# Optimization experiments

Hardware: AMD Instinct MI355X
Metric: run time of the kernel (lower is better)

## Reference

```python
import jax, jax.numpy as jnp
from jax import lax
import numpy as np

WIDTH = 3.0        # tool half-width (voxels)
SIGMA = 1.0        # soft mask edge (voxels)
BLUR_SIGMA = 1.5   # post-deposit isotropic blur sigma (voxels)
EPS = 1e-8


def _gauss_blur(x, sigma):
    """Separable Gaussian blur over the last two axes of x: [B, X, Y]."""
    radius = int(3 * sigma)
    t = jnp.arange(-radius, radius + 1, dtype=x.dtype)
    k = jnp.exp(-0.5 * (t / sigma) ** 2)
    k = k / k.sum()
    x4 = x[:, None]                      # [B,1,X,Y] NCHW
    kh = k.reshape(1, 1, -1, 1)
    x4 = lax.conv_general_dilated(x4, kh, (1, 1), 'SAME')
    kw = k.reshape(1, 1, 1, -1)
    x4 = lax.conv_general_dilated(x4, kw, (1, 1), 'SAME')
    return x4[:, 0]


def setup_inputs() -> dict:
    key = jax.random.key(0)
    k1, k2, k3 = jax.random.split(key, 3)
    B, H, W = 16, 1024, 1024
    occ = jax.random.uniform(k1, (B, H, W), dtype=jnp.float32)
    # push start/end points well inside the grid (voxel coordinates)
    action_start = jax.random.uniform(k2, (B, 3), minval=200.0, maxval=800.0, dtype=jnp.float32)
    action_end = action_start + jax.random.uniform(k3, (B, 3), minval=-150.0, maxval=150.0, dtype=jnp.float32)
    return {"occ": occ, "action_start": action_start, "action_end": action_end}


def reference(occ, action_start, action_end):
    # coordinate-convention transpose (see SplatPushModel docs)
    rho = jnp.swapaxes(occ, 1, 2)            # [B, X, Y]
    B, X, Y = rho.shape
    p0 = action_start[:, :2]                 # [B,2]
    p1 = action_end[:, :2]                   # [B,2]

    d = p1 - p0
    L = jnp.sqrt(jnp.sum(d * d, axis=-1) + EPS)      # [B] segment length
    u = d / L[:, None]                               # unit push direction
    n = jnp.stack([-u[:, 1], u[:, 0]], axis=-1)      # unit normal

    gx = jnp.arange(X, dtype=rho.dtype)[None, :, None]   # [1,X,1]
    gy = jnp.arange(Y, dtype=rho.dtype)[None, None, :]   # [1,1,Y]
    bc = lambda v: v[:, None, None]                      # [B] -> [B,1,1]

    # --- swept band: soft distance-to-segment mask ---
    rx = gx - bc(p0[:, 0])
    ry = gy - bc(p0[:, 1])
    t = jnp.clip(rx * bc(u[:, 0]) + ry * bc(u[:, 1]), 0.0, L[:, None, None])
    dx = rx - t * bc(u[:, 0])
    dy = ry - t * bc(u[:, 1])
    dist = jnp.sqrt(dx * dx + dy * dy + EPS)
    swept = jax.nn.sigmoid((WIDTH - dist) / SIGMA)       # [B,X,Y]

    m_swept = jnp.sum(rho * swept, axis=(1, 2))          # [B] mass to move
    pile_depth = m_swept / (2.0 * WIDTH)                 # [B]

    # --- landing zone probe (rectangle past p1) ---
    qx = gx - bc(p1[:, 0])
    qy = gy - bc(p1[:, 1])
    s = qx * bc(u[:, 0]) + qy * bc(u[:, 1])              # along-direction coord
    r = qx * bc(n[:, 0]) + qy * bc(n[:, 1])              # perpendicular coord
    lat = jax.nn.sigmoid((WIDTH - jnp.abs(r)) / SIGMA)
    probe = jax.nn.sigmoid(s / SIGMA) * jax.nn.sigmoid((bc(pile_depth) - s) / SIGMA) * lat
    existing = jnp.sum(rho * probe, axis=(1, 2))         # [B]
    extra = existing / (2.0 * WIDTH)                     # [B] forward extension

    # --- deposit band, shifted forward by extra_depth ---
    dep_mask = (jax.nn.sigmoid((s - bc(extra)) / SIGMA)
                * jax.nn.sigmoid((bc(extra) + bc(pile_depth) - s) / SIGMA)
                * lat)
    dep_norm = m_swept / (jnp.sum(dep_mask, axis=(1, 2)) + EPS)
    dep = dep_mask * dep_norm[:, None, None]             # mass-conserving deposit

    if BLUR_SIGMA > 0:
        dep = _gauss_blur(dep, BLUR_SIGMA)

    rho_new = rho * (1.0 - swept) + dep
    return jnp.swapaxes(rho_new, 1, 2)
```

## Files before the change

kernel.cpp:

```cpp
#include <hip/hip_runtime.h>
#include <math.h>

#define BB    16
#define HH    1024
#define WW    1024
#define EPSF  1e-8f
#define RAD   4
#define MARG  24.f
#define WMAX  128
#define FW    (WMAX + 16)
#define UNR   4

struct BlurK { float k[9]; };

__device__ __forceinline__ float sigf(float z) {
    z = fmaxf(fminf(z, 40.f), -40.f);
    return 1.f / (1.f + __expf(-z));
}

struct Geom { float p0x, p0y, p1x, p1y, L, ux, uy; };

__device__ __forceinline__ Geom load_geom(const float* as, const float* ae, int b) {
    Geom g;
    g.p0x = as[3 * b];  g.p0y = as[3 * b + 1];
    g.p1x = ae[3 * b];  g.p1y = ae[3 * b + 1];
    float dx = g.p1x - g.p0x, dy = g.p1y - g.p0y;
    g.L  = sqrtf(dx * dx + dy * dy + EPSF);
    g.ux = dx / g.L;  g.uy = dy / g.L;
    return g;
}

__device__ __forceinline__ float sweptf(const Geom& g, float x, float y) {
    float rx = x - g.p0x, ry = y - g.p0y;
    float t  = fminf(fmaxf(rx * g.ux + ry * g.uy, 0.f), g.L);
    float dx = rx - t * g.ux, dy = ry - t * g.uy;
    float dist = sqrtf(dx * dx + dy * dy + EPSF);
    return sigf(3.f - dist);
}

__device__ __forceinline__ void slat(const Geom& g, float x, float y, float& s, float& lat) {
    float qx = x - g.p1x, qy = y - g.p1y;
    s = qx * g.ux + qy * g.uy;
    float r = qx * (-g.uy) + qy * g.ux;
    lat = sigf(3.f - fabsf(r));
}

__device__ __forceinline__ void capsule_bbox(const Geom& g, float m,
                                             int& x0, int& x1, int& y0, int& y1) {
    x0 = max(0, (int)floorf(fminf(g.p0x, g.p1x) - m));
    x1 = min(WW - 1, (int)ceilf(fmaxf(g.p0x, g.p1x) + m));
    y0 = max(0, (int)floorf(fminf(g.p0y, g.p1y) - m));
    y1 = min(HH - 1, (int)ceilf(fmaxf(g.p0y, g.p1y) + m));
}

__device__ __forceinline__ void strip_bbox(const Geom& g, float s0, float s1, float m,
                                           int& x0, int& x1, int& y0, int& y1) {
    float xmin = 1e9f, xmax = -1e9f, ymin = 1e9f, ymax = -1e9f;
    #pragma unroll
    for (int i = 0; i < 4; i++) {
        float s = (i & 1) ? s1 : s0;
        float r = (i & 2) ? m : -m;
        float x = g.p1x + s * g.ux - r * g.uy;
        float y = g.p1y + s * g.uy + r * g.ux;
        xmin = fminf(xmin, x); xmax = fmaxf(xmax, x);
        ymin = fminf(ymin, y); ymax = fmaxf(ymax, y);
    }
    x0 = max(0, (int)floorf(xmin)); x1 = min(WW - 1, (int)ceilf(xmax));
    y0 = max(0, (int)floorf(ymin)); y1 = min(HH - 1, (int)ceilf(ymax));
}

__device__ __forceinline__ bool ivx(float a, float A, float B, float& lo, float& hi) {
    if (fabsf(a) < 1e-5f) return !(A > 0.f || B < 0.f);
    float l = A / a, h = B / a;
    if (a < 0.f) { float t = l; l = h; h = t; }
    lo = fmaxf(lo, l); hi = fminf(hi, h);
    return true;
}

__device__ __forceinline__ float brb1024(float v, float* sm) {
    #pragma unroll
    for (int off = 32; off > 0; off >>= 1) v += __shfl_down(v, off);
    const int lane = threadIdx.x & 63, wid = threadIdx.x >> 6;
    if (lane == 0) sm[wid] = v;
    __syncthreads();
    float r = 0.f;
    #pragma unroll
    for (int i = 0; i < 16; i++) r += sm[i];
    __syncthreads();
    return r;
}

__global__ __launch_bounds__(1024)
void k_scalars(const float* __restrict__ occ, const float* __restrict__ as,
               const float* __restrict__ ae, float* __restrict__ sc) {
    const int b = blockIdx.x, tid = threadIdx.x;
    const int tx4 = tid & 63;
    const int ty  = tid >> 6;
    __shared__ float sm[16];
    Geom g = load_geom(as, ae, b);
    const float4* src4 = (const float4*)(occ + ((size_t)b << 20));

    int x0, x1, y0, y1;

    capsule_bbox(g, MARG, x0, x1, y0, y1);
    int c0 = x0 >> 2, c1 = x1 >> 2;
    float sum = 0.f;
    for (int cc = c0; cc <= c1; cc += 64) {
        const int c = cc + tx4;
        const bool cok = (c <= c1);
        const float fx = (float)(c << 2);
        for (int y = y0 + ty; y <= y1; y += 16 * UNR) {
            float4 vv[UNR];
            #pragma unroll
            for (int j = 0; j < UNR; j++) {
                const int yy = y + 16 * j;
                vv[j] = (cok && yy <= y1) ? src4[yy * 256 + c]
                                          : make_float4(0.f, 0.f, 0.f, 0.f);
            }
            #pragma unroll
            for (int j = 0; j < UNR; j++) {
                const int yy = y + 16 * j;
                if (cok && yy <= y1) {
                    const float fy = (float)yy;
                    sum += vv[j].x * sweptf(g, fx + 0.f, fy);
                    sum += vv[j].y * sweptf(g, fx + 1.f, fy);
                    sum += vv[j].z * sweptf(g, fx + 2.f, fy);
                    sum += vv[j].w * sweptf(g, fx + 3.f, fy);
                }
            }
        }
    }
    const float m_swept = brb1024(sum, sm);
    const float pile = m_swept * (1.f / 6.f);

    strip_bbox(g, -MARG, pile + MARG, MARG, x0, x1, y0, y1);
    c0 = x0 >> 2; c1 = x1 >> 2;
    sum = 0.f;
    for (int cc = c0; cc <= c1; cc += 64) {
        const int c = cc + tx4;
        const bool cok = (c <= c1);
        const float fx = (float)(c << 2);
        for (int y = y0 + ty; y <= y1; y += 16 * UNR) {
            float4 vv[UNR];
            #pragma unroll
            for (int j = 0; j < UNR; j++) {
                const int yy = y + 16 * j;
                vv[j] = (cok && yy <= y1) ? src4[yy * 256 + c]
                                          : make_float4(0.f, 0.f, 0.f, 0.f);
            }
            #pragma unroll
            for (int j = 0; j < UNR; j++) {
                const int yy = y + 16 * j;
                if (cok && yy <= y1) {
                    const float fy = (float)yy;
                    #pragma unroll
                    for (int e = 0; e < 4; e++) {
                        float s, lat; slat(g, fx + (float)e, fy, s, lat);
                        sum += (&vv[j].x)[e] * sigf(s) * sigf(pile - s) * lat;
                    }
                }
            }
        }
    }
    const float existing = brb1024(sum, sm);
    const float extra = existing * (1.f / 6.f);

    strip_bbox(g, extra - MARG, extra + pile + MARG, MARG, x0, x1, y0, y1);
    sum = 0.f;
    {
        const int tx = tid & 127, ty8 = tid >> 7;
        for (int y = y0 + ty8; y <= y1; y += 8) {
            const float fy = (float)y;
            for (int x = x0 + tx; x <= x1; x += 128) {
                float s, lat; slat(g, (float)x, fy, s, lat);
                sum += sigf(s - extra) * sigf(extra + pile - s) * lat;
            }
        }
    }
    const float summask = brb1024(sum, sm);

    if (tid == 0) {
        sc[b * 4 + 0] = pile;
        sc[b * 4 + 1] = extra;
        sc[b * 4 + 2] = m_swept / (summask + EPSF);
    }
}

__global__ __launch_bounds__(256)
void k_fused(const float* __restrict__ occ, const float* __restrict__ as,
             const float* __restrict__ ae, const float* __restrict__ sc,
             float* __restrict__ out, BlurK wk) {
    const int b = blockIdx.y, bx = blockIdx.x, tid = threadIdx.x;
    const float pile     = sc[b * 4 + 0];
    const float extra    = sc[b * 4 + 1];
    const float dep_norm = sc[b * 4 + 2];
    Geom g = load_geom(as, ae, b);

    const size_t ibase = (size_t)b << 20;
    const float4* src = (const float4*)(occ + ibase);
    float4*       dst = (float4*)(out + ibase);
    const int yb = bx * 8;
    const int base4 = bx * 2048 + tid;

    float4 v[8];
    #pragma unroll
    for (int k = 0; k < 8; k++) v[k] = src[base4 + k * 256];

    int cx0, cx1, cy0, cy1; capsule_bbox(g, MARG, cx0, cx1, cy0, cy1);
    const int x = tid << 2;
    if (x + 3 >= cx0 && x <= cx1) {
        #pragma unroll
        for (int k = 0; k < 8; k++) {
            const int y = yb + k;
            if (y >= cy0 && y <= cy1) {
                const float fy = (float)y, fx = (float)x;
                v[k].x *= 1.f - sweptf(g, fx + 0.f, fy);
                v[k].y *= 1.f - sweptf(g, fx + 1.f, fy);
                v[k].z *= 1.f - sweptf(g, fx + 2.f, fy);
                v[k].w *= 1.f - sweptf(g, fx + 3.f, fy);
            }
        }
    }

    int sx0, sx1, sy0, sy1;
    strip_bbox(g, extra - MARG, extra + pile + MARG, MARG, sx0, sx1, sy0, sy1);

    __shared__ float draw[16][FW];
    __shared__ float hb[16][WMAX];

    if (yb + 7 >= sy0 && yb <= sy1) {
        const float sA = extra - MARG, sB = extra + pile + MARG;
        float xlo = 1e9f, xhi = -1e9f;
        #pragma unroll
        for (int r = 0; r < 16; r++) {
            const float dy = (float)(yb - RAD + r) - g.p1y;
            float lo = -1e9f, hi = 1e9f;
            bool ok = ivx(g.ux, sA - dy * g.uy, sB - dy * g.uy, lo, hi);
            ok = ok && ivx(-g.uy, -MARG - dy * g.ux, MARG - dy * g.ux, lo, hi);
            if (ok && lo <= hi) { xlo = fminf(xlo, lo); xhi = fmaxf(xhi, hi); }
        }
        const int csx0 = max(sx0, (int)floorf(xlo + g.p1x));
        const int csx1 = min(sx1, (int)ceilf(xhi + g.p1x));

        if (csx0 <= csx1) {
            const int cxa = csx0 & ~3;
            for (int cx = cxa; cx <= csx1; cx += WMAX) {
                const int w = min(WMAX, csx1 - cx + 1);

                for (int i = tid; i < 16 * FW; i += 256) {
                    const int ly = i / FW, lx = i - ly * FW;
                    if (lx < w + 8) {
                        const int gy = yb - RAD + ly, gx = cx - RAD + lx;
                        float val = 0.f;
                        if ((unsigned)gx < WW && (unsigned)gy < HH) {
                            float s, lat; slat(g, (float)gx, (float)gy, s, lat);
                            val = sigf(s - extra) * sigf(extra + pile - s) * lat * dep_norm;
                        }
                        draw[ly][lx] = val;
                    }
                }
                __syncthreads();

                for (int i = tid; i < 16 * WMAX; i += 256) {
                    const int ly = i >> 7, lx = i & 127;
                    if (lx < w) {
                        float acc = 0.f;
                        #pragma unroll
                        for (int j = 0; j < 9; j++) acc += wk.k[j] * draw[ly][lx + j];
                        hb[ly][lx] = acc;
                    }
                }
                __syncthreads();

                for (int i = tid; i < 8 * WMAX; i += 256) {
                    const int k = i >> 7, lx = i & 127;
                    if (lx < w) {
                        float acc = 0.f;
                        #pragma unroll
                        for (int j = 0; j < 9; j++) acc += wk.k[j] * hb[k + j][lx];
                        draw[k][lx] = acc;
                    }
                }
                __syncthreads();

                const int lx0 = (tid << 2) - cx;
                if (lx0 >= 0 && lx0 < w) {
                    if (lx0 + 3 < w) {
                        #pragma unroll
                        for (int k = 0; k < 8; k++) {
                            const float4 vb = *(const float4*)&draw[k][lx0];
                            v[k].x += vb.x; v[k].y += vb.y; v[k].z += vb.z; v[k].w += vb.w;
                        }
                    } else {
                        #pragma unroll
                        for (int k = 0; k < 8; k++)
                            for (int e = 0; e < 4; e++)
                                if (lx0 + e < w) (&v[k].x)[e] += draw[k][lx0 + e];
                    }
                }
                __syncthreads();
            }
        }
    }

    #pragma unroll
    for (int k = 0; k < 8; k++) dst[base4 + k * 256] = v[k];
}

extern "C" void kernel_launch(void* const* d_in, const int* in_sizes, int n_in,
                              void* d_out, int out_size, void* d_ws, size_t ws_size,
                              hipStream_t stream) {
    const float* occ = (const float*)d_in[0];
    const float* as  = (const float*)d_in[1];
    const float* ae  = (const float*)d_in[2];
    float* out = (float*)d_out;
    float* sc  = (float*)d_ws;

    BlurK wk;
    {
        float s = 0.f;
        for (int i = 0; i < 9; i++) {
            float t = (float)(i - RAD) / 1.5f;
            wk.k[i] = expf(-0.5f * t * t);
            s += wk.k[i];
        }
        for (int i = 0; i < 9; i++) wk.k[i] /= s;
    }

    k_scalars<<<dim3(BB), 1024, 0, stream>>>(occ, as, ae, sc);
    k_fused  <<<dim3(HH / 8, BB), 256, 0, stream>>>(occ, as, ae, sc, out, wk);
}
```

Measured before the change: 163.3 us.

## Fuse swept-mass reduction into streaming pass and split deposit into sparse kernel

The main streaming kernel now copies occ to out, applies the swept mask, and produces per-block partial sums of swept mass in the same pass. This removes the serial swept-mass reduction from the 16-block scalar kernel, which now only runs the probe and mask-sum phases. The blur and deposit move to a separate small kernel that adds into out only over the strip bbox tiles. The cost is an extra launch and a read-modify-write of the deposit region in global memory.

```diff
diff --git a/kernel.cpp b/kernel.cpp
--- a/kernel.cpp
+++ b/kernel.cpp
@@ -7,6 +7,8 @@
 #define EPSF  1e-8f
 #define RAD   4
 #define MARG  24.f
+#define NB1   128
+#define NB3   32
 #define WMAX  128
 #define FW    (WMAX + 16)
 #define UNR   4
@@ -77,6 +79,17 @@
     return true;
 }
 
+__device__ __forceinline__ float brb256(float v, float* sm) {
+    #pragma unroll
+    for (int off = 32; off > 0; off >>= 1) v += __shfl_down(v, off);
+    const int lane = threadIdx.x & 63, wid = threadIdx.x >> 6;
+    if (lane == 0) sm[wid] = v;
+    __syncthreads();
+    float r = sm[0] + sm[1] + sm[2] + sm[3];
+    __syncthreads();
+    return r;
+}
+
 __device__ __forceinline__ float brb1024(float v, float* sm) {
     #pragma unroll
     for (int off = 32; off > 0; off >>= 1) v += __shfl_down(v, off);
@@ -90,9 +103,53 @@
     return r;
 }
 
+__global__ __launch_bounds__(256)
+void k_main(const float* __restrict__ occ, const float* __restrict__ as,
+            const float* __restrict__ ae, float* __restrict__ out,
+            float* __restrict__ part1) {
+    const int b = blockIdx.y, bx = blockIdx.x, tid = threadIdx.x;
+    Geom g = load_geom(as, ae, b);
+    const size_t ibase = (size_t)b << 20;
+    const float4* src = (const float4*)(occ + ibase);
+    float4*       dst = (float4*)(out + ibase);
+    const int yb = bx * 8;
+    const int base4 = bx * 2048 + tid;
+
+    float4 v[8];
+    #pragma unroll
+    for (int k = 0; k < 8; k++) v[k] = src[base4 + k * 256];
+
+    int cx0, cx1, cy0, cy1; capsule_bbox(g, MARG, cx0, cx1, cy0, cy1);
+    const int x = tid << 2;
+    float msum = 0.f;
+    if (x + 3 >= cx0 && x <= cx1) {
+        #pragma unroll
+        for (int k = 0; k < 8; k++) {
+            const int y = yb + k;
+            if (y >= cy0 && y <= cy1) {
+                const float fy = (float)y, fx = (float)x;
+                const float s0 = sweptf(g, fx + 0.f, fy);
+                const float s1 = sweptf(g, fx + 1.f, fy);
+                const float s2 = sweptf(g, fx + 2.f, fy);
+                const float s3 = sweptf(g, fx + 3.f, fy);
+                msum += v[k].x * s0 + v[k].y * s1 + v[k].z * s2 + v[k].w * s3;
+                v[k].x *= 1.f - s0; v[k].y *= 1.f - s1;
+                v[k].z *= 1.f - s2; v[k].w *= 1.f - s3;
+            }
+        }
+    }
+    #pragma unroll
+    for (int k = 0; k < 8; k++) dst[base4 + k * 256] = v[k];
+
+    __shared__ float sm[4];
+    const float bs = brb256(msum, sm);
+    if (tid == 0) part1[b * NB1 + bx] = bs;
+}
+
 __global__ __launch_bounds__(1024)
-void k_scalars(const float* __restrict__ occ, const float* __restrict__ as,
-               const float* __restrict__ ae, float* __restrict__ sc) {
+void k_probe(const float* __restrict__ occ, const float* __restrict__ as,
+             const float* __restrict__ ae, const float* __restrict__ part1,
+             float* __restrict__ sc) {
     const int b = blockIdx.x, tid = threadIdx.x;
     const int tx4 = tid & 63;
     const int ty  = tid >> 6;
@@ -100,9 +157,11 @@
     Geom g = load_geom(as, ae, b);
     const float4* src4 = (const float4*)(occ + ((size_t)b << 20));
 
+    const float m_swept = brb1024((tid < NB1) ? part1[b * NB1 + tid] : 0.f, sm);
+    const float pile = m_swept * (1.f / 6.f);
+
     int x0, x1, y0, y1;
-
-    capsule_bbox(g, MARG, x0, x1, y0, y1);
+    strip_bbox(g, -MARG, pile + MARG, MARG, x0, x1, y0, y1);
     int c0 = x0 >> 2, c1 = x1 >> 2;
     float sum = 0.f;
     for (int cc = c0; cc <= c1; cc += 64) {
@@ -122,37 +181,6 @@
                 const int yy = y + 16 * j;
                 if (cok && yy <= y1) {
                     const float fy = (float)yy;
-                    sum += vv[j].x * sweptf(g, fx + 0.f, fy);
-                    sum += vv[j].y * sweptf(g, fx + 1.f, fy);
-                    sum += vv[j].z * sweptf(g, fx + 2.f, fy);
-                    sum += vv[j].w * sweptf(g, fx + 3.f, fy);
-                }
-            }
-        }
-    }
-    const float m_swept = brb1024(sum, sm);
-    const float pile = m_swept * (1.f / 6.f);
-
-    strip_bbox(g, -MARG, pile + MARG, MARG, x0, x1, y0, y1);
-    c0 = x0 >> 2; c1 = x1 >> 2;
-    sum = 0.f;
-    for (int cc = c0; cc <= c1; cc += 64) {
-        const int c = cc + tx4;
-        const bool cok = (c <= c1);
-        const float fx = (float)(c << 2);
-        for (int y = y0 + ty; y <= y1; y += 16 * UNR) {
-            float4 vv[UNR];
-            #pragma unroll
-            for (int j = 0; j < UNR; j++) {
-                const int yy = y + 16 * j;
-                vv[j] = (cok && yy <= y1) ? src4[yy * 256 + c]
-                                          : make_float4(0.f, 0.f, 0.f, 0.f);
-            }
-            #pragma unroll
-            for (int j = 0; j < UNR; j++) {
-                const int yy = y + 16 * j;
-                if (cok && yy <= y1) {
-                    const float fy = (float)yy;
                     #pragma unroll
                     for (int e = 0; e < 4; e++) {
                         float s, lat; slat(g, fx + (float)e, fy, s, lat);
@@ -187,53 +215,32 @@
 }
 
 __global__ __launch_bounds__(256)
-void k_fused(const float* __restrict__ occ, const float* __restrict__ as,
-             const float* __restrict__ ae, const float* __restrict__ sc,
-             float* __restrict__ out, BlurK wk) {
+void k_dep(const float* __restrict__ as, const float* __restrict__ ae,
+           const float* __restrict__ sc, float* __restrict__ out, BlurK wk) {
     const int b = blockIdx.y, bx = blockIdx.x, tid = threadIdx.x;
     const float pile     = sc[b * 4 + 0];
     const float extra    = sc[b * 4 + 1];
     const float dep_norm = sc[b * 4 + 2];
     Geom g = load_geom(as, ae, b);
 
-    const size_t ibase = (size_t)b << 20;
-    const float4* src = (const float4*)(occ + ibase);
-    float4*       dst = (float4*)(out + ibase);
-    const int yb = bx * 8;
-    const int base4 = bx * 2048 + tid;
-
-    float4 v[8];
-    #pragma unroll
-    for (int k = 0; k < 8; k++) v[k] = src[base4 + k * 256];
-
-    int cx0, cx1, cy0, cy1; capsule_bbox(g, MARG, cx0, cx1, cy0, cy1);
-    const int x = tid << 2;
-    if (x + 3 >= cx0 && x <= cx1) {
-        #pragma unroll
-        for (int k = 0; k < 8; k++) {
-            const int y = yb + k;
-            if (y >= cy0 && y <= cy1) {
-                const float fy = (float)y, fx = (float)x;
-                v[k].x *= 1.f - sweptf(g, fx + 0.f, fy);
-                v[k].y *= 1.f - sweptf(g, fx + 1.f, fy);
-                v[k].z *= 1.f - sweptf(g, fx + 2.f, fy);
-                v[k].w *= 1.f - sweptf(g, fx + 3.f, fy);
-            }
-        }
-    }
-
     int sx0, sx1, sy0, sy1;
     strip_bbox(g, extra - MARG, extra + pile + MARG, MARG, sx0, sx1, sy0, sy1);
+    if (sx0 > sx1 || sy0 > sy1) return;
+    float* outb = out + ((size_t)b << 20);
 
     __shared__ float draw[16][FW];
     __shared__ float hb[16][WMAX];
 
-    if (yb + 7 >= sy0 && yb <= sy1) {
-        const float sA = extra - MARG, sB = extra + pile + MARG;
+    const int nty = (sy1 - sy0) / 8 + 1;
+    const float sA = extra - MARG, sB = extra + pile + MARG;
+
+    for (int ty = bx; ty < nty; ty += NB3) {
+        const int yt = sy0 + ty * 8;
+
         float xlo = 1e9f, xhi = -1e9f;
         #pragma unroll
         for (int r = 0; r < 16; r++) {
-            const float dy = (float)(yb - RAD + r) - g.p1y;
+            const float dy = (float)(yt - RAD + r) - g.p1y;
             float lo = -1e9f, hi = 1e9f;
             bool ok = ivx(g.ux, sA - dy * g.uy, sB - dy * g.uy, lo, hi);
             ok = ok && ivx(-g.uy, -MARG - dy * g.ux, MARG - dy * g.ux, lo, hi);
@@ -241,70 +248,56 @@
         }
         const int csx0 = max(sx0, (int)floorf(xlo + g.p1x));
         const int csx1 = min(sx1, (int)ceilf(xhi + g.p1x));
-
-        if (csx0 <= csx1) {
-            const int cxa = csx0 & ~3;
-            for (int cx = cxa; cx <= csx1; cx += WMAX) {
-                const int w = min(WMAX, csx1 - cx + 1);
-
-                for (int i = tid; i < 16 * FW; i += 256) {
-                    const int ly = i / FW, lx = i - ly * FW;
-                    if (lx < w + 8) {
-                        const int gy = yb - RAD + ly, gx = cx - RAD + lx;
-                        float val = 0.f;
-                        if ((unsigned)gx < WW && (unsigned)gy < HH) {
-                            float s, lat; slat(g, (float)gx, (float)gy, s, lat);
-                            val = sigf(s - extra) * sigf(extra + pile - s) * lat * dep_norm;
-                        }
-                        draw[ly][lx] = val;
+        if (csx0 > csx1) continue;
+
+        for (int cx = csx0 & ~3; cx <= csx1; cx += WMAX) {
+            const int w = min(WMAX, csx1 - cx + 1);
+
+            for (int i = tid; i < 16 * FW; i += 256) {
+                const int ly = i / FW, lx = i - ly * FW;
+                if (lx < w + 8) {
+                    const int gy = yt - RAD + ly, gx = cx - RAD + lx;
+                    float val = 0.f;
+                    if ((unsigned)gx < WW && (unsigned)gy < HH) {
+                        float s, lat; slat(g, (float)gx, (float)gy, s, lat);
+                        val = sigf(s - extra) * sigf(extra + pile - s) * lat * dep_norm;
                     }
+                    draw[ly][lx] = val;
                 }
-                __syncthreads();
-
-                for (int i = tid; i < 16 * WMAX; i += 256) {
-                    const int ly = i >> 7, lx = i & 127;
-                    if (lx < w) {
-                        float acc = 0.f;
-                        #pragma unroll
-                        for (int j = 0; j < 9; j++) acc += wk.k[j] * draw[ly][lx + j];
-                        hb[ly][lx] = acc;
-                    }
+            }
+            __syncthreads();
+
+            for (int i = tid; i < 16 * WMAX; i += 256) {
+                const int ly = i >> 7, lx = i & 127;
+                if (lx < w) {
+                    float acc = 0.f;
+                    #pragma unroll
+                    for (int j = 0; j < 9; j++) acc += wk.k[j] * draw[ly][lx + j];
+                    hb[ly][lx] = acc;
                 }
-                __syncthreads();
-
-                for (int i = tid; i < 8 * WMAX; i += 256) {
-                    const int k = i >> 7, lx = i & 127;
-                    if (lx < w) {
-                        float acc = 0.f;
-                        #pragma unroll
-                        for (int j = 0; j < 9; j++) acc += wk.k[j] * hb[k + j][lx];
-                        draw[k][lx] = acc;
-                    }
+            }
+            __syncthreads();
+
+            for (int i = tid; i < 8 * WMAX; i += 256) {
+                const int k = i >> 7, lx = i & 127;
+                if (lx < w) {
+                    float acc = 0.f;
+                    #pragma unroll
+                    for (int j = 0; j < 9; j++) acc += wk.k[j] * hb[k + j][lx];
+                    draw[k][lx] = acc;
                 }
-                __syncthreads();
-
-                const int lx0 = (tid << 2) - cx;
-                if (lx0 >= 0 && lx0 < w) {
-                    if (lx0 + 3 < w) {
-                        #pragma unroll
-                        for (int k = 0; k < 8; k++) {
-                            const float4 vb = *(const float4*)&draw[k][lx0];
-                            v[k].x += vb.x; v[k].y += vb.y; v[k].z += vb.z; v[k].w += vb.w;
-                        }
-                    } else {
-                        #pragma unroll
-                        for (int k = 0; k < 8; k++)
-                            for (int e = 0; e < 4; e++)
-                                if (lx0 + e < w) (&v[k].x)[e] += draw[k][lx0 + e];
-                    }
-                }
-                __syncthreads();
-            }
-        }
-    }
-
-    #pragma unroll
-    for (int k = 0; k < 8; k++) dst[base4 + k * 256] = v[k];
+            }
+            __syncthreads();
+
+            for (int i = tid; i < 8 * WMAX; i += 256) {
+                const int k = i >> 7, lx = i & 127;
+                const int gy = yt + k, gx = cx + lx;
+                if (lx < w && (unsigned)gy < HH && (unsigned)gx < WW)
+                    outb[((size_t)gy << 10) + gx] += draw[k][lx];
+            }
+            __syncthreads();
+        }
+    }
 }
 
 extern "C" void kernel_launch(void* const* d_in, const int* in_sizes, int n_in,
@@ -313,8 +306,9 @@
     const float* occ = (const float*)d_in[0];
     const float* as  = (const float*)d_in[1];
     const float* ae  = (const float*)d_in[2];
-    float* out = (float*)d_out;
-    float* sc  = (float*)d_ws;
+    float* out   = (float*)d_out;
+    float* part1 = (float*)d_ws;
+    float* sc    = part1 + BB * NB1;
 
     BlurK wk;
     {
@@ -327,6 +321,7 @@
         for (int i = 0; i < 9; i++) wk.k[i] /= s;
     }
 
-    k_scalars<<<dim3(BB), 1024, 0, stream>>>(occ, as, ae, sc);
-    k_fused  <<<dim3(HH / 8, BB), 256, 0, stream>>>(occ, as, ae, sc, out, wk);
-}
+    k_main <<<dim3(NB1, BB), 256,  0, stream>>>(occ, as, ae, out, part1);
+    k_probe<<<dim3(BB),      1024, 0, stream>>>(occ, as, ae, part1, sc);
+    k_dep  <<<dim3(NB3, BB), 256,  0, stream>>>(as, ae, sc, out, wk);
+}
```

Measured after the change: 158.8 us. 2.8% less time.
